# Kernel tuning notes

Hardware: AMD Instinct MI355X
Metric: run time of the kernel (lower is better)

Reference implementation:

```python
import jax, jax.numpy as jnp
import numpy as np

EPS = 1e-5

def layer_norm(x, w, b):
    mu = jnp.mean(x, axis=-1, keepdims=True)
    var = jnp.var(x, axis=-1, keepdims=True)
    return (x - mu) * jax.lax.rsqrt(var + EPS) * w + b

def setup_inputs() -> dict:
    key = jax.random.key(0)
    ks = jax.random.split(key, 9)
    B, N, d, hidden = 1, 512, 64, 128
    s = 0.02
    return {
        "z": jax.random.normal(ks[0], (B, N, N, d), dtype=jnp.float32),
        "ln_in_w": jnp.ones((d,), jnp.float32),
        "ln_in_b": jnp.zeros((d,), jnp.float32),
        "Wp": jax.random.normal(ks[1], (d, 2 * hidden), jnp.float32) * s,
        "Wg": jax.random.normal(ks[2], (d, 2 * hidden), jnp.float32) * s,
        "ln_out_w": jnp.ones((hidden,), jnp.float32),
        "ln_out_b": jnp.zeros((hidden,), jnp.float32),
        "Wout": jax.random.normal(ks[3], (hidden, d), jnp.float32) * s,
        "Wgate": jax.random.normal(ks[4], (d, d), jnp.float32) * s,
    }

def reference(z, ln_in_w, ln_in_b, Wp, Wg, ln_out_w, ln_out_b, Wout, Wgate):
    # z: [B, N, N, d]
    h = layer_norm(z, ln_in_w, ln_in_b)
    p = h @ Wp                               # [B,N,N,2*hidden]
    g_in = jax.nn.sigmoid(h @ Wg)            # [B,N,N,2*hidden]
    pg = p * g_in
    a, b = jnp.split(pg, 2, axis=-1)         # each [B,N,N,hidden]
    # direction == 'outgoing'
    out = jnp.einsum('bikd,bjkd->bijd', a, b)  # [B,N,N,hidden]
    out = layer_norm(out, ln_out_w, ln_out_b)
    g_out = jax.nn.sigmoid(h @ Wgate)        # [B,N,N,d]
    return (out @ Wout) * g_out              # [B,N,N,d]
```

## Files before the change

kernel.cpp:

```cpp
#include <hip/hip_runtime.h>
#include <hip/hip_fp16.h>


typedef _Float16 half_t;
typedef _Float16 f16x4 __attribute__((ext_vector_type(4)));
typedef _Float16 f16x8 __attribute__((ext_vector_type(8)));
typedef float f32x4 __attribute__((ext_vector_type(4)));

#define NSEQ 512
#define HID 128
#define ROWS (NSEQ * NSEQ)

#define GLOAD16(src, dst)                                                        \
    __builtin_amdgcn_global_load_lds(                                            \
        (const __attribute__((address_space(1))) void*)(src),                    \
        (__attribute__((address_space(3))) void*)(dst), 16, 0, 0)

__device__ __forceinline__ float fast_sigmoid(float x) {
    float e = __builtin_amdgcn_exp2f(-1.44269504088896f * x);
    return __builtin_amdgcn_rcpf(1.f + e);
}

__global__ void k_prep_w(const float* __restrict__ Wp, const float* __restrict__ Wg,
                         const float* __restrict__ Wgate,
                         const float* __restrict__ ln_out_w, const float* __restrict__ ln_out_b,
                         const float* __restrict__ Wout,
                         half_t* __restrict__ Wimg, half_t* __restrict__ W1t,
                         float* __restrict__ s1, float* __restrict__ s2) {
    int bid = blockIdx.x, t = threadIdx.x;
    if (bid < 18) {
        int chunk = bid * 256 + t;
        int ch = chunk >= 2304;
        int q = chunk - ch * 2304;
        int lr = q >> 3, slot = q & 7;
        int co = slot ^ (lr & 7);
        int grow;
        if (lr < 128)      grow = ch * 128 + lr;
        else if (lr < 256) grow = 256 + ch * 128 + (lr - 128);
        else               grow = 512 + ch * 32 + (lr - 256);
        f16x8 vals;
        #pragma unroll
        for (int j = 0; j < 8; ++j) {
            int l = co * 8 + j;
            float v;
            if (grow < 256)      v = Wp[l * 256 + grow];
            else if (grow < 512) v = Wg[l * 256 + (grow - 256)];
            else                 v = Wgate[l * 64 + (grow - 512)];
            vals[j] = (half_t)v;
        }
        *(f16x8*)(Wimg + (size_t)chunk * 8) = vals;
    } else {
        #pragma unroll
        for (int i = 0; i < 32; ++i) {
            int idx = t * 32 + i;
            int o = idx >> 7, c = idx & 127;
            W1t[idx] = (half_t)(ln_out_w[c] * Wout[c * 64 + o]);
        }
        if (t < 64) {
            float a1 = 0.f, a2 = 0.f;
            for (int c = 0; c < 128; ++c) {
                float wo = Wout[c * 64 + t];
                a1 += ln_out_w[c] * wo;
                a2 += ln_out_b[c] * wo;
            }
            s1[t] = a1; s2[t] = a2;
        }
    }
}

__global__ __launch_bounds__(256) void k_ln_in(const float* __restrict__ z,
                                               const float* __restrict__ w,
                                               const float* __restrict__ b,
                                               half_t* __restrict__ h) {
    int t = threadIdx.x;
    int row = blockIdx.x * 16 + (t >> 4);
    int c4 = t & 15;
    f32x4 x = *(const f32x4*)(z + (size_t)row * 64 + c4 * 4);
    float s = x[0] + x[1] + x[2] + x[3];
    float s2 = x[0]*x[0] + x[1]*x[1] + x[2]*x[2] + x[3]*x[3];
    #pragma unroll
    for (int off = 1; off < 16; off <<= 1) {
        s  += __shfl_xor(s,  off, 64);
        s2 += __shfl_xor(s2, off, 64);
    }
    float mu = s * (1.f / 64.f);
    float var = s2 * (1.f / 64.f) - mu * mu;
    float rs = rsqrtf(var + 1e-5f);
    f32x4 wv = *(const f32x4*)(w + c4 * 4);
    f32x4 bv = *(const f32x4*)(b + c4 * 4);
    f16x4 o;
    #pragma unroll
    for (int j = 0; j < 4; ++j)
        o[j] = (half_t)((x[j] - mu) * rs * wv[j] + bv[j]);
    *(f16x4*)(h + (size_t)row * 64 + c4 * 4) = o;
}

__global__ __launch_bounds__(256) void k_proj(const half_t* __restrict__ h,
                                              const half_t* __restrict__ Wimg,
                                              half_t* __restrict__ a_t,
                                              half_t* __restrict__ b_t,
                                              half_t* __restrict__ g_out) {
    __shared__ half_t Wl[288 * 64];

    int t = threadIdx.x;
    int ch = blockIdx.y;
    int bx = blockIdx.x;
    int r0 = bx * 64;
    int wid = t >> 6, lane = t & 63;
    int m = lane & 15, g = lane >> 4;

    const half_t* wsrc = Wimg + (size_t)ch * 2304 * 8;
    #pragma unroll
    for (int it = 0; it < 9; ++it) {
        int cb = it * 256 + wid * 64;
        GLOAD16(wsrc + (size_t)(cb + lane) * 8, Wl + (size_t)cb * 8);
    }

    int growbase = r0 + wid * 16;
    f16x8 af[2];
    #pragma unroll
    for (int ks = 0; ks < 2; ++ks)
        af[ks] = *(const f16x8*)(h + (size_t)(growbase + m) * 64 + ks * 32 + g * 8);

    __syncthreads();

    half_t* dst = (ch == 0) ? a_t : b_t;
    int swz = (bx >> 4) & 3;
    int r8 = wid * 2 + (g >> 1);
    int dk = (r8 & 4) | ((r8 & 3) ^ swz);
    size_t rowoff = (size_t)r0 + dk * 8 + (g & 1) * 4;

    #pragma unroll
    for (int pt = 0; pt < 8; ++pt) {
        f32x4 accp = {0.f, 0.f, 0.f, 0.f}, accg = {0.f, 0.f, 0.f, 0.f};
        #pragma unroll
        for (int ks = 0; ks < 2; ++ks) {
            int kb = (ks * 32 + g * 8) * 2;
            int lrp = pt * 16 + m;
            f16x8 bp = *(const f16x8*)((char*)Wl + lrp * 128 + (kb ^ ((lrp & 7) << 4)));
            int lrg = 128 + pt * 16 + m;
            f16x8 bg = *(const f16x8*)((char*)Wl + lrg * 128 + (kb ^ ((lrg & 7) << 4)));
            accp = __builtin_amdgcn_mfma_f32_16x16x32_f16(af[ks], bp, accp, 0, 0, 0);
            accg = __builtin_amdgcn_mfma_f32_16x16x32_f16(af[ks], bg, accg, 0, 0, 0);
        }
        f16x4 pk;
        #pragma unroll
        for (int r = 0; r < 4; ++r)
            pk[r] = (half_t)(accp[r] * fast_sigmoid(accg[r]));
        *(f16x4*)(dst + (size_t)(pt * 16 + m) * ROWS + rowoff) = pk;
    }

    #pragma unroll
    for (int gt = 0; gt < 2; ++gt) {
        f32x4 acc = {0.f, 0.f, 0.f, 0.f};
        #pragma unroll
        for (int ks = 0; ks < 2; ++ks) {
            int kb = (ks * 32 + g * 8) * 2;
            int lr = 256 + gt * 16 + m;
            f16x8 bb = *(const f16x8*)((char*)Wl + lr * 128 + (kb ^ ((lr & 7) << 4)));
            acc = __builtin_amdgcn_mfma_f32_16x16x32_f16(af[ks], bb, acc, 0, 0, 0);
        }
        int och = ch * 32 + gt * 16 + m;
        #pragma unroll
        for (int r = 0; r < 4; ++r) {
            float og = fast_sigmoid(acc[r]);
            int grow = growbase + g * 4 + r;
            g_out[(size_t)grow * 64 + och] = (half_t)og;
        }
    }
}

#define EBUF 8192
__global__ __launch_bounds__(256) void k_einsum(const half_t* __restrict__ a_t,
                                                const half_t* __restrict__ b_t,
                                                half_t* __restrict__ out_mid) {
    __shared__ half_t lds[3 * EBUF];

    int t = threadIdx.x;
    int wid = t >> 6, lane = t & 63;
    int m = lane & 15, g = lane >> 4;

    int bid = blockIdx.x;
    int xcd = bid & 7;
    int rest = bid >> 3;
    int gen = rest >> 6;
    int local = rest & 63;
    int c = xcd + 8 * (gen * 4 + (local >> 4));
    int tile = local & 15;
    int i0 = (tile >> 2) * 128, j0 = (tile & 3) * 128;

    const half_t* A = a_t + (size_t)c * ROWS;
    const half_t* B = b_t + (size_t)c * ROWS;
    int wr = wid >> 1, wc = wid & 1;

    f32x4 acc[4][4] = {};

#define STAGE_A(ktt, base, it)                                                    \
    {                                                                             \
        int cb = (it) * 256 + wid * 64;              \
        int chunk = cb + lane;                                                    \
        GLOAD16(A + (size_t)(i0 + (chunk >> 2)) * 512 + (ktt) * 32 + (chunk & 3) * 8, \
                (base) + (size_t)cb * 8);                                         \
    }
#define STAGE_B(ktt, base, it)                                                    \
    {                                                                             \
        int cb = (it) * 256 + wid * 64;                                           \
        int chunk = cb + lane;                                                    \
        GLOAD16(B + (size_t)(j0 + (chunk >> 2)) * 512 + (ktt) * 32 + (chunk & 3) * 8, \
                (base) + 4096 + (size_t)cb * 8);                                  \
    }
#define STAGE_ALL(ktt, base)                                                      \
    STAGE_A(ktt, base, 0) STAGE_A(ktt, base, 1) STAGE_B(ktt, base, 0) STAGE_B(ktt, base, 1)

    STAGE_ALL(0, lds)
    STAGE_ALL(1, lds + EBUF)

    #pragma unroll
    for (int kt = 0; kt < 16; ++kt) {
        const half_t* Ac = lds + (kt % 3) * EBUF;
        const half_t* Bc = Ac + 4096;
        half_t* nxt = lds + ((kt + 2) % 3) * EBUF;

        if (kt <= 14) asm volatile("s_waitcnt vmcnt(4)" ::: "memory");
        else          asm volatile("s_waitcnt vmcnt(0)" ::: "memory");
        __builtin_amdgcn_s_barrier();
        __builtin_amdgcn_sched_barrier(0);

        f16x8 bf[4];
        #pragma unroll
        for (int ni = 0; ni < 4; ++ni) {
            int lrow = wc * 64 + ni * 16 + m;
            bf[ni] = *(const f16x8*)((const char*)Bc + lrow * 64 +
                                     ((g ^ ((lrow >> 1) & 3)) << 4));
        }
        #pragma unroll
        for (int mi = 0; mi < 4; ++mi) {
            int lrow = wr * 64 + mi * 16 + m;
            f16x8 afr = *(const f16x8*)((const char*)Ac + lrow * 64 +
                                        ((g ^ ((lrow >> 1) & 3)) << 4));
            if (kt < 14) {
                if (mi == 0)      STAGE_A(kt + 2, nxt, 0)
                else if (mi == 1) STAGE_A(kt + 2, nxt, 1)
                else if (mi == 2) STAGE_B(kt + 2, nxt, 0)
                else              STAGE_B(kt + 2, nxt, 1)
            }
            __builtin_amdgcn_s_setprio(1);
            #pragma unroll
            for (int ni = 0; ni < 4; ++ni)
                acc[mi][ni] = __builtin_amdgcn_mfma_f32_16x16x32_f16(afr, bf[ni], acc[mi][ni], 0, 0, 0);
            __builtin_amdgcn_s_setprio(0);
        }
    }
#undef STAGE_ALL
#undef STAGE_B
#undef STAGE_A

    half_t* O = out_mid + (size_t)c * ROWS;
    #pragma unroll
    for (int mi = 0; mi < 4; ++mi) {
        #pragma unroll
        for (int ni = 0; ni < 4; ++ni) {
            int row = i0 + wr * 64 + mi * 16 + g * 4;
            int col = j0 + wc * 64 + ni * 16 + m;
            #pragma unroll
            for (int r2 = 0; r2 < 4; ++r2)
                O[(size_t)(row + r2) * 512 + col] = (half_t)acc[mi][ni][r2];
        }
    }
}

__global__ __launch_bounds__(256) void k_final(const half_t* __restrict__ out_mid,
                                               const half_t* __restrict__ W1t,
                                               const float* __restrict__ s1g,
                                               const float* __restrict__ s2g,
                                               const half_t* __restrict__ g_out,
                                               float* __restrict__ out) {
    __shared__ half_t midl[128 * 64];
    __shared__ half_t midt[64 * 128];
    __shared__ half_t w1l[64 * 128];
    __shared__ half_t gl[64 * 72];
    __shared__ float smu[64], srs[64], s1l[64], s2l[64];

    int t = threadIdx.x;
    int pos0 = blockIdx.x * 64;

    #pragma unroll
    for (int it = 0; it < 4; ++it) {
        int chunk = it * 256 + t;
        int cc = chunk >> 3, co = chunk & 7;
        *(uint4*)((char*)midl + cc * 128 + co * 16) =
            *(const uint4*)(out_mid + (size_t)cc * ROWS + pos0 + co * 8);
    }
    #pragma unroll
    for (int it = 0; it < 4; ++it) {
        int chunk = it * 256 + t;
        int row = chunk >> 4, slot = chunk & 15;
        *(uint4*)((char*)w1l + row * 256 + ((slot * 16) ^ ((row & 7) << 4))) =
            *(const uint4*)(W1t + row * 128 + slot * 8);
    }
    #pragma unroll
    for (int it = 0; it < 2; ++it) {
        int chunk = it * 256 + t;
        int row = chunk >> 3, co = chunk & 7;
        *(uint4*)((char*)gl + row * 144 + co * 16) =
            *(const uint4*)(g_out + (size_t)(pos0 + row) * 64 + co * 8);
    }
    if (t < 64) { s1l[t] = s1g[t]; s2l[t] = s2g[t]; }
    __syncthreads();

    {
        int p = t >> 2, q = t & 3;
        float s = 0.f, s2 = 0.f;
        #pragma unroll
        for (int cc4 = 0; cc4 < 4; ++cc4) {
            f16x8 pack;
            #pragma unroll
            for (int j = 0; j < 8; ++j) {
                half_t hv = midl[(q * 32 + cc4 * 8 + j) * 64 + p];
                float v = (float)hv;
                s += v; s2 += v * v;
                pack[j] = hv;
            }
            int slot = q * 4 + cc4;
            *(f16x8*)((char*)midt + p * 256 + ((slot * 16) ^ ((p & 7) << 4))) = pack;
        }
        s  += __shfl_xor(s, 1, 64);  s  += __shfl_xor(s, 2, 64);
        s2 += __shfl_xor(s2, 1, 64); s2 += __shfl_xor(s2, 2, 64);
        if (q == 0) {
            float mu = s * (1.f / 128.f);
            float var = s2 * (1.f / 128.f) - mu * mu;
            smu[p] = mu;
            srs[p] = rsqrtf(var + 1e-5f);
        }
    }
    __syncthreads();

    int wid = t >> 6, lane = t & 63;
    int m = lane & 15, g = lane >> 4;

    f32x4 acc[4] = {};
    #pragma unroll
    for (int ks = 0; ks < 4; ++ks) {
        int arow = wid * 16 + m;
        f16x8 af = *(const f16x8*)((char*)midt + arow * 256 +
                                   (((4 * ks + g) * 16) ^ ((arow & 7) << 4)));
        #pragma unroll
        for (int ni = 0; ni < 4; ++ni) {
            int brow = ni * 16 + m;
            f16x8 bf = *(const f16x8*)((char*)w1l + brow * 256 +
                                       (((4 * ks + g) * 16) ^ ((brow & 7) << 4)));
            acc[ni] = __builtin_amdgcn_mfma_f32_16x16x32_f16(af, bf, acc[ni], 0, 0, 0);
        }
    }

    #pragma unroll
    for (int ni = 0; ni < 4; ++ni) {
        int o = ni * 16 + m;
        float v1 = s1l[o], v2 = s2l[o];
        #pragma unroll
        for (int r = 0; r < 4; ++r) {
            int lrow = wid * 16 + g * 4 + r;
            float mu = smu[lrow], rs = srs[lrow];
            float val = acc[ni][r] * rs - mu * rs * v1 + v2;
            float gate = (float)gl[lrow * 72 + o];
            out[(size_t)(pos0 + lrow) * 64 + o] = val * gate;
        }
    }
}

extern "C" void kernel_launch(void* const* d_in, const int* in_sizes, int n_in,
                              void* d_out, int out_size, void* d_ws, size_t ws_size,
                              hipStream_t stream) {
    const float* z        = (const float*)d_in[0];
    const float* ln_in_w  = (const float*)d_in[1];
    const float* ln_in_b  = (const float*)d_in[2];
    const float* Wp       = (const float*)d_in[3];
    const float* Wg       = (const float*)d_in[4];
    const float* ln_out_w = (const float*)d_in[5];
    const float* ln_out_b = (const float*)d_in[6];
    const float* Wout     = (const float*)d_in[7];
    const float* Wgate    = (const float*)d_in[8];
    float* out = (float*)d_out;

    char* wsb = (char*)d_ws;
    half_t* Wimg = (half_t*)wsb;
    half_t* W1t  = (half_t*)(wsb + 81920);
    float*  s1   = (float*)(wsb + 98304);
    float*  s2   = (float*)(wsb + 98560);
    half_t* a_t  = (half_t*)(wsb + 131072);
    half_t* b_t  = a_t + (size_t)HID * ROWS;
    half_t* gout = b_t + (size_t)HID * ROWS;
    half_t* omid = gout + (size_t)ROWS * 64;
    half_t* h    = omid;

    k_prep_w<<<dim3(19), dim3(256), 0, stream>>>(Wp, Wg, Wgate, ln_out_w, ln_out_b, Wout,
                                                 Wimg, W1t, s1, s2);
    k_ln_in<<<dim3(ROWS / 16), dim3(256), 0, stream>>>(z, ln_in_w, ln_in_b, h);
    k_proj<<<dim3(ROWS / 64, 2), dim3(256), 0, stream>>>(h, Wimg, a_t, b_t, gout);
    k_einsum<<<dim3(2048), dim3(256), 0, stream>>>(a_t, b_t, omid);
    k_final<<<dim3(ROWS / 64), dim3(256), 0, stream>>>(omid, W1t, s1, s2, gout, out);
}
```

Baseline: 172.5 us.

## Stage proj outputs through LDS and restructure GEMM main loop into two-phase ping-pong

The projection kernel now collects each gated p*g tile in a padded LDS buffer and writes it to the transposed a_t/b_t arrays as 16-byte coalesced chunks instead of scattered 8-byte stores. The triangle GEMM main loop is split into two half-phases, each loading A fragments, issuing its share of global-to-LDS prefetches, then running a barrier-separated MFMA cluster. The wait for the next stage moves to the end of the iteration. The aim is better store coalescing and tighter interleaving of loads with MFMAs across waves, at the cost of extra barriers and LDS traffic.

```diff
diff --git a/kernel.cpp b/kernel.cpp
--- a/kernel.cpp
+++ b/kernel.cpp
@@ -101,6 +101,7 @@
                                               half_t* __restrict__ b_t,
                                               half_t* __restrict__ g_out) {
     __shared__ half_t Wl[288 * 64];
+    __shared__ half_t pgl[64 * 66];
 
     int t = threadIdx.x;
     int ch = blockIdx.y;
@@ -126,31 +127,40 @@
 
     half_t* dst = (ch == 0) ? a_t : b_t;
     int swz = (bx >> 4) & 3;
-    int r8 = wid * 2 + (g >> 1);
-    int dk = (r8 & 4) | ((r8 & 3) ^ swz);
-    size_t rowoff = (size_t)r0 + dk * 8 + (g & 1) * 4;
-
-    #pragma unroll
-    for (int pt = 0; pt < 8; ++pt) {
-        f32x4 accp = {0.f, 0.f, 0.f, 0.f}, accg = {0.f, 0.f, 0.f, 0.f};
-        #pragma unroll
-        for (int ks = 0; ks < 2; ++ks) {
-            int kb = (ks * 32 + g * 8) * 2;
-            int lrp = pt * 16 + m;
-            f16x8 bp = *(const f16x8*)((char*)Wl + lrp * 128 + (kb ^ ((lrp & 7) << 4)));
-            int lrg = 128 + pt * 16 + m;
-            f16x8 bg = *(const f16x8*)((char*)Wl + lrg * 128 + (kb ^ ((lrg & 7) << 4)));
-            accp = __builtin_amdgcn_mfma_f32_16x16x32_f16(af[ks], bp, accp, 0, 0, 0);
-            accg = __builtin_amdgcn_mfma_f32_16x16x32_f16(af[ks], bg, accg, 0, 0, 0);
-        }
-        f16x4 pk;
-        #pragma unroll
-        for (int r = 0; r < 4; ++r)
-            pk[r] = (half_t)(accp[r] * fast_sigmoid(accg[r]));
-        *(f16x4*)(dst + (size_t)(pt * 16 + m) * ROWS + rowoff) = pk;
-    }
-
-    #pragma unroll
+
+    for (int grp = 0; grp < 2; ++grp) {
+        #pragma unroll
+        for (int pt4 = 0; pt4 < 4; ++pt4) {
+            int pt = grp * 4 + pt4;
+            f32x4 accp = {0.f, 0.f, 0.f, 0.f}, accg = {0.f, 0.f, 0.f, 0.f};
+            #pragma unroll
+            for (int ks = 0; ks < 2; ++ks) {
+                int kb = (ks * 32 + g * 8) * 2;
+                int lrp = pt * 16 + m;
+                f16x8 bp = *(const f16x8*)((char*)Wl + lrp * 128 + (kb ^ ((lrp & 7) << 4)));
+                int lrg = 128 + pt * 16 + m;
+                f16x8 bg = *(const f16x8*)((char*)Wl + lrg * 128 + (kb ^ ((lrg & 7) << 4)));
+                accp = __builtin_amdgcn_mfma_f32_16x16x32_f16(af[ks], bp, accp, 0, 0, 0);
+                accg = __builtin_amdgcn_mfma_f32_16x16x32_f16(af[ks], bg, accg, 0, 0, 0);
+            }
+            f16x4 pk;
+            #pragma unroll
+            for (int r = 0; r < 4; ++r)
+                pk[r] = (half_t)(accp[r] * fast_sigmoid(accg[r]));
+            *(f16x4*)&pgl[(pt4 * 16 + m) * 66 + wid * 16 + g * 4] = pk;
+        }
+        __syncthreads();
+        #pragma unroll
+        for (int it = 0; it < 2; ++it) {
+            int chunk = it * 256 + t;
+            int cl = chunk >> 3, r8 = chunk & 7;
+            f16x8 v = *(const f16x8*)&pgl[cl * 66 + r8 * 8];
+            int dk = (r8 & 4) | ((r8 & 3) ^ swz);
+            *(f16x8*)(dst + (size_t)(grp * 64 + cl) * ROWS + r0 + dk * 8) = v;
+        }
+        __syncthreads();
+    }
+
     for (int gt = 0; gt < 2; ++gt) {
         f32x4 acc = {0.f, 0.f, 0.f, 0.f};
         #pragma unroll
@@ -209,11 +219,12 @@
         GLOAD16(B + (size_t)(j0 + (chunk >> 2)) * 512 + (ktt) * 32 + (chunk & 3) * 8, \
                 (base) + 4096 + (size_t)cb * 8);                                  \
     }
-#define STAGE_ALL(ktt, base)                                                      \
-    STAGE_A(ktt, base, 0) STAGE_A(ktt, base, 1) STAGE_B(ktt, base, 0) STAGE_B(ktt, base, 1)
-
-    STAGE_ALL(0, lds)
-    STAGE_ALL(1, lds + EBUF)
+
+    STAGE_A(0, lds, 0) STAGE_A(0, lds, 1) STAGE_B(0, lds, 0) STAGE_B(0, lds, 1)
+    STAGE_A(1, lds + EBUF, 0) STAGE_A(1, lds + EBUF, 1)
+    STAGE_B(1, lds + EBUF, 0) STAGE_B(1, lds + EBUF, 1)
+    asm volatile("s_waitcnt vmcnt(4)" ::: "memory");
+    __builtin_amdgcn_s_barrier();
 
     #pragma unroll
     for (int kt = 0; kt < 16; ++kt) {
@@ -221,11 +232,6 @@
         const half_t* Bc = Ac + 4096;
         half_t* nxt = lds + ((kt + 2) % 3) * EBUF;
 
-        if (kt <= 14) asm volatile("s_waitcnt vmcnt(4)" ::: "memory");
-        else          asm volatile("s_waitcnt vmcnt(0)" ::: "memory");
-        __builtin_amdgcn_s_barrier();
-        __builtin_amdgcn_sched_barrier(0);
-
         f16x8 bf[4];
         #pragma unroll
         for (int ni = 0; ni < 4; ++ni) {
@@ -233,25 +239,46 @@
             bf[ni] = *(const f16x8*)((const char*)Bc + lrow * 64 +
                                      ((g ^ ((lrow >> 1) & 3)) << 4));
         }
-        #pragma unroll
-        for (int mi = 0; mi < 4; ++mi) {
-            int lrow = wr * 64 + mi * 16 + m;
-            f16x8 afr = *(const f16x8*)((const char*)Ac + lrow * 64 +
-                                        ((g ^ ((lrow >> 1) & 3)) << 4));
-            if (kt < 14) {
-                if (mi == 0)      STAGE_A(kt + 2, nxt, 0)
-                else if (mi == 1) STAGE_A(kt + 2, nxt, 1)
-                else if (mi == 2) STAGE_B(kt + 2, nxt, 0)
-                else              STAGE_B(kt + 2, nxt, 1)
-            }
-            __builtin_amdgcn_s_setprio(1);
-            #pragma unroll
-            for (int ni = 0; ni < 4; ++ni)
-                acc[mi][ni] = __builtin_amdgcn_mfma_f32_16x16x32_f16(afr, bf[ni], acc[mi][ni], 0, 0, 0);
-            __builtin_amdgcn_s_setprio(0);
-        }
-    }
-#undef STAGE_ALL
+        int lr0 = wr * 64 + m;
+        f16x8 af0 = *(const f16x8*)((const char*)Ac + lr0 * 64 +
+                                    ((g ^ ((lr0 >> 1) & 3)) << 4));
+        int lr1 = lr0 + 16;
+        f16x8 af1 = *(const f16x8*)((const char*)Ac + lr1 * 64 +
+                                    ((g ^ ((lr1 >> 1) & 3)) << 4));
+        if (kt < 14) { STAGE_A(kt + 2, nxt, 0) STAGE_A(kt + 2, nxt, 1) }
+        __builtin_amdgcn_s_barrier();
+        asm volatile("s_waitcnt lgkmcnt(0)" ::: "memory");
+        __builtin_amdgcn_sched_barrier(0);
+        __builtin_amdgcn_s_setprio(1);
+        #pragma unroll
+        for (int ni = 0; ni < 4; ++ni) {
+            acc[0][ni] = __builtin_amdgcn_mfma_f32_16x16x32_f16(af0, bf[ni], acc[0][ni], 0, 0, 0);
+            acc[1][ni] = __builtin_amdgcn_mfma_f32_16x16x32_f16(af1, bf[ni], acc[1][ni], 0, 0, 0);
+        }
+        __builtin_amdgcn_s_setprio(0);
+
+        int lr2 = lr0 + 32;
+        f16x8 af2 = *(const f16x8*)((const char*)Ac + lr2 * 64 +
+                                    ((g ^ ((lr2 >> 1) & 3)) << 4));
+        int lr3 = lr0 + 48;
+        f16x8 af3 = *(const f16x8*)((const char*)Ac + lr3 * 64 +
+                                    ((g ^ ((lr3 >> 1) & 3)) << 4));
+        if (kt < 14) { STAGE_B(kt + 2, nxt, 0) STAGE_B(kt + 2, nxt, 1) }
+        __builtin_amdgcn_s_barrier();
+        asm volatile("s_waitcnt lgkmcnt(0)" ::: "memory");
+        __builtin_amdgcn_sched_barrier(0);
+        __builtin_amdgcn_s_setprio(1);
+        #pragma unroll
+        for (int ni = 0; ni < 4; ++ni) {
+            acc[2][ni] = __builtin_amdgcn_mfma_f32_16x16x32_f16(af2, bf[ni], acc[2][ni], 0, 0, 0);
+            acc[3][ni] = __builtin_amdgcn_mfma_f32_16x16x32_f16(af3, bf[ni], acc[3][ni], 0, 0, 0);
+        }
+        __builtin_amdgcn_s_setprio(0);
+
+        if (kt <= 13) asm volatile("s_waitcnt vmcnt(4)" ::: "memory");
+        else          asm volatile("s_waitcnt vmcnt(0)" ::: "memory");
+        __builtin_amdgcn_s_barrier();
+    }
 #undef STAGE_B
 #undef STAGE_A
 
```

Result: faster. 159.7 us (-7.4%).

## Stage proj output through LDS for coalesced stores; load einsum A directly to registers

Applied to the files above, without the earlier changes.

In k_proj, gated projection results are first written to a padded LDS tile and then stored to global memory as 16-byte coalesced chunks, replacing scattered 8-byte transposed stores. In k_einsum, the A operand is no longer staged through LDS. Each wave loads its A fragments straight from global memory into double-buffered registers, keeping the swizzled addressing. Only B stays in a triple-buffered LDS ring, which cuts LDS use so launch bounds can request 3 blocks per CU. The trade-offs are more vector registers, uncoalesced per-lane A loads with redundant reads across waves, and extra barriers in k_proj.

```diff
diff --git a/kernel.cpp b/kernel.cpp
--- a/kernel.cpp
+++ b/kernel.cpp
@@ -101,6 +101,7 @@
                                               half_t* __restrict__ b_t,
                                               half_t* __restrict__ g_out) {
     __shared__ half_t Wl[288 * 64];
+    __shared__ half_t pgl[64 * 66];
 
     int t = threadIdx.x;
     int ch = blockIdx.y;
@@ -126,31 +127,40 @@
 
     half_t* dst = (ch == 0) ? a_t : b_t;
     int swz = (bx >> 4) & 3;
-    int r8 = wid * 2 + (g >> 1);
-    int dk = (r8 & 4) | ((r8 & 3) ^ swz);
-    size_t rowoff = (size_t)r0 + dk * 8 + (g & 1) * 4;
-
-    #pragma unroll
-    for (int pt = 0; pt < 8; ++pt) {
-        f32x4 accp = {0.f, 0.f, 0.f, 0.f}, accg = {0.f, 0.f, 0.f, 0.f};
-        #pragma unroll
-        for (int ks = 0; ks < 2; ++ks) {
-            int kb = (ks * 32 + g * 8) * 2;
-            int lrp = pt * 16 + m;
-            f16x8 bp = *(const f16x8*)((char*)Wl + lrp * 128 + (kb ^ ((lrp & 7) << 4)));
-            int lrg = 128 + pt * 16 + m;
-            f16x8 bg = *(const f16x8*)((char*)Wl + lrg * 128 + (kb ^ ((lrg & 7) << 4)));
-            accp = __builtin_amdgcn_mfma_f32_16x16x32_f16(af[ks], bp, accp, 0, 0, 0);
-            accg = __builtin_amdgcn_mfma_f32_16x16x32_f16(af[ks], bg, accg, 0, 0, 0);
-        }
-        f16x4 pk;
-        #pragma unroll
-        for (int r = 0; r < 4; ++r)
-            pk[r] = (half_t)(accp[r] * fast_sigmoid(accg[r]));
-        *(f16x4*)(dst + (size_t)(pt * 16 + m) * ROWS + rowoff) = pk;
-    }
-
-    #pragma unroll
+
+    for (int grp = 0; grp < 2; ++grp) {
+        #pragma unroll
+        for (int pt4 = 0; pt4 < 4; ++pt4) {
+            int pt = grp * 4 + pt4;
+            f32x4 accp = {0.f, 0.f, 0.f, 0.f}, accg = {0.f, 0.f, 0.f, 0.f};
+            #pragma unroll
+            for (int ks = 0; ks < 2; ++ks) {
+                int kb = (ks * 32 + g * 8) * 2;
+                int lrp = pt * 16 + m;
+                f16x8 bp = *(const f16x8*)((char*)Wl + lrp * 128 + (kb ^ ((lrp & 7) << 4)));
+                int lrg = 128 + pt * 16 + m;
+                f16x8 bg = *(const f16x8*)((char*)Wl + lrg * 128 + (kb ^ ((lrg & 7) << 4)));
+                accp = __builtin_amdgcn_mfma_f32_16x16x32_f16(af[ks], bp, accp, 0, 0, 0);
+                accg = __builtin_amdgcn_mfma_f32_16x16x32_f16(af[ks], bg, accg, 0, 0, 0);
+            }
+            f16x4 pk;
+            #pragma unroll
+            for (int r = 0; r < 4; ++r)
+                pk[r] = (half_t)(accp[r] * fast_sigmoid(accg[r]));
+            *(f16x4*)&pgl[(pt4 * 16 + m) * 66 + wid * 16 + g * 4] = pk;
+        }
+        __syncthreads();
+        #pragma unroll
+        for (int it = 0; it < 2; ++it) {
+            int chunk = it * 256 + t;
+            int cl = chunk >> 3, r8 = chunk & 7;
+            f16x8 v = *(const f16x8*)&pgl[cl * 66 + r8 * 8];
+            int dk = (r8 & 4) | ((r8 & 3) ^ swz);
+            *(f16x8*)(dst + (size_t)(grp * 64 + cl) * ROWS + r0 + dk * 8) = v;
+        }
+        __syncthreads();
+    }
+
     for (int gt = 0; gt < 2; ++gt) {
         f32x4 acc = {0.f, 0.f, 0.f, 0.f};
         #pragma unroll
@@ -170,11 +180,11 @@
     }
 }
 
-#define EBUF 8192
-__global__ __launch_bounds__(256) void k_einsum(const half_t* __restrict__ a_t,
-                                                const half_t* __restrict__ b_t,
-                                                half_t* __restrict__ out_mid) {
-    __shared__ half_t lds[3 * EBUF];
+#define BBUF 4096
+__global__ __launch_bounds__(256, 3) void k_einsum(const half_t* __restrict__ a_t,
+                                                   const half_t* __restrict__ b_t,
+                                                   half_t* __restrict__ out_mid) {
+    __shared__ half_t ldsB[3 * BBUF];
 
     int t = threadIdx.x;
     int wid = t >> 6, lane = t & 63;
@@ -195,37 +205,41 @@
 
     f32x4 acc[4][4] = {};
 
-#define STAGE_A(ktt, base, it)                                                    \
+    const half_t* aaddr[4];
+    #pragma unroll
+    for (int mi = 0; mi < 4; ++mi) {
+        int row = i0 + wr * 64 + mi * 16 + m;
+        int slot = g ^ ((row >> 1) & 3);
+        aaddr[mi] = A + (size_t)row * 512 + slot * 8;
+    }
+
+#define STAGE_B(ktt, it)                                                          \
     {                                                                             \
         int cb = (it) * 256 + wid * 64;              \
         int chunk = cb + lane;                                                    \
-        GLOAD16(A + (size_t)(i0 + (chunk >> 2)) * 512 + (ktt) * 32 + (chunk & 3) * 8, \
-                (base) + (size_t)cb * 8);                                         \
-    }
-#define STAGE_B(ktt, base, it)                                                    \
-    {                                                                             \
-        int cb = (it) * 256 + wid * 64;                                           \
-        int chunk = cb + lane;                                                    \
         GLOAD16(B + (size_t)(j0 + (chunk >> 2)) * 512 + (ktt) * 32 + (chunk & 3) * 8, \
-                (base) + 4096 + (size_t)cb * 8);                                  \
-    }
-#define STAGE_ALL(ktt, base)                                                      \
-    STAGE_A(ktt, base, 0) STAGE_A(ktt, base, 1) STAGE_B(ktt, base, 0) STAGE_B(ktt, base, 1)
-
-    STAGE_ALL(0, lds)
-    STAGE_ALL(1, lds + EBUF)
+                ldsB + ((ktt) % 3) * BBUF + (size_t)cb * 8);                      \
+    }
+
+    f16x8 areg[2][4];
+    #pragma unroll
+    for (int mi = 0; mi < 4; ++mi)
+        areg[0][mi] = *(const f16x8*)(aaddr[mi]);
+    STAGE_B(0, 0) STAGE_B(0, 1)
+    STAGE_B(1, 0) STAGE_B(1, 1)
 
     #pragma unroll
     for (int kt = 0; kt < 16; ++kt) {
-        const half_t* Ac = lds + (kt % 3) * EBUF;
-        const half_t* Bc = Ac + 4096;
-        half_t* nxt = lds + ((kt + 2) % 3) * EBUF;
-
-        if (kt <= 14) asm volatile("s_waitcnt vmcnt(4)" ::: "memory");
-        else          asm volatile("s_waitcnt vmcnt(0)" ::: "memory");
+        if (kt < 15) {
+            #pragma unroll
+            for (int mi = 0; mi < 4; ++mi)
+                areg[(kt + 1) & 1][mi] = *(const f16x8*)(aaddr[mi] + (kt + 1) * 32);
+        }
+        if (kt < 15) asm volatile("s_waitcnt vmcnt(6)" ::: "memory");
+        else         asm volatile("s_waitcnt vmcnt(0)" ::: "memory");
         __builtin_amdgcn_s_barrier();
-        __builtin_amdgcn_sched_barrier(0);
-
+
+        const half_t* Bc = ldsB + (kt % 3) * BBUF;
         f16x8 bf[4];
         #pragma unroll
         for (int ni = 0; ni < 4; ++ni) {
@@ -233,27 +247,19 @@
             bf[ni] = *(const f16x8*)((const char*)Bc + lrow * 64 +
                                      ((g ^ ((lrow >> 1) & 3)) << 4));
         }
-        #pragma unroll
-        for (int mi = 0; mi < 4; ++mi) {
-            int lrow = wr * 64 + mi * 16 + m;
-            f16x8 afr = *(const f16x8*)((const char*)Ac + lrow * 64 +
-                                        ((g ^ ((lrow >> 1) & 3)) << 4));
-            if (kt < 14) {
-                if (mi == 0)      STAGE_A(kt + 2, nxt, 0)
-                else if (mi == 1) STAGE_A(kt + 2, nxt, 1)
-                else if (mi == 2) STAGE_B(kt + 2, nxt, 0)
-                else              STAGE_B(kt + 2, nxt, 1)
-            }
-            __builtin_amdgcn_s_setprio(1);
+        if (kt < 14) { STAGE_B(kt + 2, 0) STAGE_B(kt + 2, 1) }
+        asm volatile("s_waitcnt lgkmcnt(0)" ::: "memory");
+        __builtin_amdgcn_sched_barrier(0);
+        __builtin_amdgcn_s_setprio(1);
+        #pragma unroll
+        for (int mi = 0; mi < 4; ++mi)
             #pragma unroll
             for (int ni = 0; ni < 4; ++ni)
-                acc[mi][ni] = __builtin_amdgcn_mfma_f32_16x16x32_f16(afr, bf[ni], acc[mi][ni], 0, 0, 0);
-            __builtin_amdgcn_s_setprio(0);
-        }
-    }
-#undef STAGE_ALL
+                acc[mi][ni] = __builtin_amdgcn_mfma_f32_16x16x32_f16(
+                    areg[kt & 1][mi], bf[ni], acc[mi][ni], 0, 0, 0);
+        __builtin_amdgcn_s_setprio(0);
+    }
 #undef STAGE_B
-#undef STAGE_A
 
     half_t* O = out_mid + (size_t)c * ROWS;
     #pragma unroll
```

New measurement: 167.3 us (median of 4 runs). 3.0% less time.
